# Optimization experiments

Hardware: AMD Instinct MI355X
Metric: run time of the kernel (lower is better)

The kernel has to match this reference:

```python
import jax, jax.numpy as jnp
import numpy as np
from jax import lax

# dims per init_kwargs / input_specs
V, D, N, W, B, T = 32000, 512, 250000, 64, 4, 1024
LOOPS, THRESH = 4, 0.99


def _ln(x, scale, bias):
    m = jnp.mean(x, -1, keepdims=True)
    v = jnp.var(x, -1, keepdims=True)
    return (x - m) * lax.rsqrt(v + 1e-5) * scale + bias


def setup_inputs() -> dict:
    key = jax.random.key(0)
    ks = jax.random.split(key, 12)
    s = 0.02
    p = lambda k, shape: jax.random.normal(k, shape, jnp.float32) * s
    return {
        "input_ids": jax.random.randint(ks[0], (B, T), 0, V),
        "embed": p(ks[1], (V, D)),
        "enc_w": p(ks[2], (D, D)), "enc_b": jnp.zeros((D,), jnp.float32),
        "ln_enc_s": jnp.ones((D,), jnp.float32), "ln_enc_b": jnp.zeros((D,), jnp.float32),
        "idx_w": p(ks[3], (D, D)), "idx_b": jnp.zeros((D,), jnp.float32),
        "mu_w": p(ks[4], (D, 1)), "mu_b": jnp.zeros((1,), jnp.float32),
        "sig_w": p(ks[5], (D, 1)), "sig_b": jnp.zeros((1,), jnp.float32),
        "pool_table": p(ks[6], (N, D)),
        "int_w1": p(ks[7], (2 * D, D)), "int_b1": jnp.zeros((D,), jnp.float32),
        "int_w2": p(ks[8], (D, D)), "int_b2": jnp.zeros((D,), jnp.float32),
        "ln_s": jnp.ones((D,), jnp.float32), "ln_b": jnp.zeros((D,), jnp.float32),
        "halt_w": p(ks[9], (D, 1)), "halt_b": jnp.zeros((1,), jnp.float32),
        "dec_w": p(ks[10], (D, V)), "dec_b": jnp.zeros((V,), jnp.float32),
    }


def reference(input_ids, embed, enc_w, enc_b, ln_enc_s, ln_enc_b,
              idx_w, idx_b, mu_w, mu_b, sig_w, sig_b, pool_table,
              int_w1, int_b1, int_w2, int_b2, ln_s, ln_b,
              halt_w, halt_b, dec_w, dec_b):
    # TinyController.encode: embed -> Dense -> gelu -> LayerNorm
    hidden = _ln(jax.nn.gelu(embed[input_ids] @ enc_w + enc_b), ln_enc_s, ln_enc_b)  # [B,T,D]
    state = hidden
    dt = hidden.dtype
    halt_prob = jnp.zeros((B, T, 1), dt)
    halted = jnp.zeros((B, T, 1), dt)
    idxs = []
    for _ in range(LOOPS):  # fixed small loop count, unrolled
        prev = state
        pooled = jnp.mean(state, axis=1)                       # [B,D]
        h = jax.nn.gelu(pooled @ idx_w + idx_b)
        mu = jax.nn.sigmoid(h @ mu_w + mu_b)                   # [B,1], coord in [0,1]
        sigma = jax.nn.softplus(h @ sig_w + sig_b) + 1e-4      # [B,1]
        # CoordinateMassivePool: contiguous window of W rows around mu*N
        center = mu[:, 0] * N
        start = jnp.clip(jnp.floor(center - W / 2).astype(jnp.int32), 0, N - W)  # [B]
        window = jax.vmap(lambda s: lax.dynamic_slice(pool_table, (s, 0), (W, D)))(start)  # [B,W,D]
        pos = (start[:, None] + jnp.arange(W)[None, :]).astype(dt) / N            # [B,W]
        w = jnp.exp(-0.5 * ((pos - mu) / sigma) ** 2)
        w = w / jnp.sum(w, axis=-1, keepdims=True)
        retrieved = jnp.einsum('bw,bwd->bd', w, window)        # [B,D]
        combined = jnp.concatenate(
            [state, jnp.broadcast_to(retrieved[:, None, :], (B, T, D))], axis=-1)  # [B,T,2D]
        integrated = _ln(jax.nn.gelu(combined @ int_w1 + int_b1) @ int_w2 + int_b2, ln_s, ln_b)
        candidate = state + integrated
        # ACT halting
        p_halt = jax.nn.sigmoid(candidate @ halt_w + halt_b)   # [B,T,1]
        halt_prob = halt_prob + p_halt * (1.0 - halted)
        new_halted = (halt_prob > THRESH).astype(dt)
        state = (1.0 - halted) * candidate + halted * prev
        halted = new_halted
        idxs.append(start)
    logits = state @ dec_w + dec_b                             # [B,T,V]
    all_indices = jnp.stack(idxs, axis=1)                      # [B,LOOPS]
    return logits, all_indices
```

## Files before the change

kernel.cpp:

```cpp
#include <hip/hip_runtime.h>

#define DEV __device__ __forceinline__

typedef __attribute__((ext_vector_type(8))) short bf16x8;
typedef __attribute__((ext_vector_type(4))) float f32x4;

typedef const __attribute__((address_space(1))) void* gsrc_t;
typedef __attribute__((address_space(3))) void* gdst_t;

DEV void gld16(const void* g, void* l){ __builtin_amdgcn_global_load_lds((gsrc_t)g,(gdst_t)l,16,0,0); }

DEV unsigned short f2bf(float f){
  union { float f; unsigned int u; } x; x.f = f;
  unsigned int u = x.u;
  return (unsigned short)((u + 0x7fffu + ((u >> 16) & 1u)) >> 16);
}
DEV unsigned long long pack4bf(float a, float b, float c, float d){
  return (unsigned long long)f2bf(a)
       | ((unsigned long long)f2bf(b) << 16)
       | ((unsigned long long)f2bf(c) << 32)
       | ((unsigned long long)f2bf(d) << 48);
}
DEV float gelu_t(float x){
  float u = 0.7978845608028654f * (x + 0.044715f * x * x * x);
  return 0.5f * x * (1.0f + tanhf(u));
}
DEV float sigmoidf_(float x){ return 1.0f / (1.0f + expf(-x)); }

DEV void BAR_TOP(){ __builtin_amdgcn_s_barrier(); asm volatile("" ::: "memory"); }
DEV void BAR_END(){
  __builtin_amdgcn_sched_barrier(0);
  asm volatile("s_waitcnt lgkmcnt(0)" ::: "memory");
  __builtin_amdgcn_s_barrier();
  asm volatile("" ::: "memory");
}

__global__ __launch_bounds__(256) void kPrep(const float* __restrict__ dec_w,
                                             unsigned short* __restrict__ dec_wT,
                                             const float* __restrict__ s0, const float* __restrict__ s1,
                                             const float* __restrict__ s2,
                                             unsigned short* __restrict__ d0, unsigned short* __restrict__ d1,
                                             unsigned short* __restrict__ d2,
                                             const int* __restrict__ ids,
                                             const float* __restrict__ embed,
                                             unsigned short* __restrict__ E){
  __shared__ float t[64][65];
  const int bid = blockIdx.x, tid = threadIdx.x;
  if (bid < 4000){
    int n0 = (bid % 500) * 64, k0 = (bid / 500) * 64;
    #pragma unroll
    for (int i = 0; i < 16; i++){
      int idx = i * 256 + tid; int r = idx >> 6, c = idx & 63;
      t[r][c] = dec_w[(size_t)(k0 + r) * 32000 + n0 + c];
    }
    __syncthreads();
    #pragma unroll
    for (int i = 0; i < 16; i++){
      int idx = i * 256 + tid; int r = idx >> 6, c = idx & 63;
      dec_wT[(size_t)(n0 + r) * 512 + k0 + c] = f2bf(t[c][r]);
    }
  } else if (bid < 4192){
    int rel = bid - 4000;
    int z = rel >> 6, rem = rel & 63;
    const float* W = (z == 0) ? s0 : (z == 1) ? s1 : s2;
    unsigned short* D = (z == 0) ? d0 : (z == 1) ? d1 : d2;
    int n0 = (rem & 7) * 64, k0 = (rem >> 3) * 64;
    #pragma unroll
    for (int i = 0; i < 16; i++){
      int idx = i * 256 + tid; int r = idx >> 6, c = idx & 63;
      t[r][c] = W[(size_t)(k0 + r) * 512 + n0 + c];
    }
    __syncthreads();
    #pragma unroll
    for (int i = 0; i < 16; i++){
      int idx = i * 256 + tid; int r = idx >> 6, c = idx & 63;
      D[(size_t)(n0 + r) * 512 + k0 + c] = f2bf(t[c][r]);
    }
  } else {
    int idx = bid - 4192;
    int row = idx * 2 + (tid >> 7);
    int t2  = tid & 127;
    int id = ids[row];
    float4 v = ((const float4*)(embed + (size_t)id * 512))[t2];
    *(unsigned long long*)(E + (size_t)row * 512 + t2 * 4) = pack4bf(v.x, v.y, v.z, v.w);
  }
}

template<int ENC>
__global__ __launch_bounds__(512) void kGemmLN(
    const unsigned short* __restrict__ A, const unsigned short* __restrict__ BT,
    const float* __restrict__ bias, const float* __restrict__ lns, const float* __restrict__ lnb,
    const float* __restrict__ hw, const float* __restrict__ hb,
    float* __restrict__ st, unsigned short* __restrict__ stb,
    float* __restrict__ part, float* __restrict__ halt_p, float* __restrict__ halted){
  __shared__ alignas(16) unsigned short lA[2][16 * 32];
  __shared__ alignas(16) unsigned short lB[2][512 * 32];
  __shared__ float pS[8][16], pQ[8][16], pH[8][16];
  __shared__ float sMean[16], sRs[16], sFac[16];
  const int tid = threadIdx.x, w = tid >> 6, lane = tid & 63;
  const int q = lane >> 4, c = lane & 15, lk8 = q * 8;
  const int r0 = blockIdx.x * 16;
  const int br = tid >> 2, bk = (tid & 3) * 8;
  f32x4 acc[4] = {};

  auto STAGE = [&](int buf, int k0){
    if (w == 0)
      gld16(A + (size_t)(r0 + (lane >> 2)) * 512 + k0 + (lane & 3) * 8, &lA[buf][lane * 8]);
    #pragma unroll
    for (int i = 0; i < 4; i++)
      gld16(BT + (size_t)(i * 128 + br) * 512 + k0 + bk, &lB[buf][(i * 512 + tid) * 8]);
  };

  STAGE(0, 0);
  #pragma unroll
  for (int t = 0; t < 16; t++){
    if (t < 15){
      STAGE((t + 1) & 1, (t + 1) * 32);
      if (w == 0) asm volatile("s_waitcnt vmcnt(5)" ::: "memory");
      else        asm volatile("s_waitcnt vmcnt(4)" ::: "memory");
    } else {
      asm volatile("s_waitcnt vmcnt(0)" ::: "memory");
    }
    BAR_TOP();
    bf16x8 af = *(const bf16x8*)&lA[t & 1][c * 32 + lk8];
    bf16x8 bfv[4];
    #pragma unroll
    for (int n = 0; n < 4; n++)
      bfv[n] = *(const bf16x8*)&lB[t & 1][(w * 64 + n * 16 + c) * 32 + lk8];
    #pragma unroll
    for (int n = 0; n < 4; n++)
      acc[n] = __builtin_amdgcn_mfma_f32_16x16x32_bf16(af, bfv[n], acc[n], 0, 0, 0);
    BAR_END();
  }

  #pragma unroll
  for (int n = 0; n < 4; n++){
    float bcol = bias[w * 64 + n * 16 + c];
    #pragma unroll
    for (int r = 0; r < 4; r++){
      float v = acc[n][r] + bcol;
      if (ENC) v = gelu_t(v);
      acc[n][r] = v;
    }
  }
  float rS[4], rQ[4];
  #pragma unroll
  for (int r = 0; r < 4; r++){
    float s = 0.f, s2 = 0.f;
    #pragma unroll
    for (int n = 0; n < 4; n++){ float v = acc[n][r]; s += v; s2 += v * v; }
    rS[r] = s; rQ[r] = s2;
  }
  #pragma unroll
  for (int mask = 1; mask < 16; mask <<= 1)
    #pragma unroll
    for (int r = 0; r < 4; r++){
      rS[r] += __shfl_xor(rS[r], mask);
      rQ[r] += __shfl_xor(rQ[r], mask);
    }
  if (c == 0)
    #pragma unroll
    for (int r = 0; r < 4; r++){ pS[w][q * 4 + r] = rS[r]; pQ[w][q * 4 + r] = rQ[r]; }
  __syncthreads();
  if (tid < 16){
    float s = 0.f, s2 = 0.f;
    #pragma unroll
    for (int v = 0; v < 8; v++){ s += pS[v][tid]; s2 += pQ[v][tid]; }
    float mean = s * (1.f / 512.f);
    float var  = s2 * (1.f / 512.f) - mean * mean;
    sMean[tid] = mean; sRs[tid] = rsqrtf(var + 1e-5f);
    if (ENC){ halt_p[r0 + tid] = 0.f; halted[r0 + tid] = 0.f; }
  }
  __syncthreads();
  float lnsv[4], lnbv[4];
  #pragma unroll
  for (int n = 0; n < 4; n++){ lnsv[n] = lns[w * 64 + n * 16 + c]; lnbv[n] = lnb[w * 64 + n * 16 + c]; }
  #pragma unroll
  for (int r = 0; r < 4; r++){
    int row = q * 4 + r;
    float mu = sMean[row], rs = sRs[row];
    #pragma unroll
    for (int n = 0; n < 4; n++)
      acc[n][r] = (acc[n][r] - mu) * rs * lnsv[n] + lnbv[n];
  }

  float sold[4][4];
  if (!ENC){
    float hwv[4];
    #pragma unroll
    for (int n = 0; n < 4; n++) hwv[n] = hw[w * 64 + n * 16 + c];
    #pragma unroll
    for (int r = 0; r < 4; r++){
      int row = q * 4 + r;
      #pragma unroll
      for (int n = 0; n < 4; n++)
        sold[n][r] = st[(size_t)(r0 + row) * 512 + w * 64 + n * 16 + c];
    }
    float rH[4];
    #pragma unroll
    for (int r = 0; r < 4; r++){
      float d = 0.f;
      #pragma unroll
      for (int n = 0; n < 4; n++) d += (sold[n][r] + acc[n][r]) * hwv[n];
      rH[r] = d;
    }
    #pragma unroll
    for (int mask = 1; mask < 16; mask <<= 1)
      #pragma unroll
      for (int r = 0; r < 4; r++) rH[r] += __shfl_xor(rH[r], mask);
    if (c == 0)
      #pragma unroll
      for (int r = 0; r < 4; r++) pH[w][q * 4 + r] = rH[r];
    __syncthreads();
    if (tid < 16){
      float d = 0.f;
      #pragma unroll
      for (int v = 0; v < 8; v++) d += pH[v][tid];
      float hd = halted[r0 + tid];
      float p  = sigmoidf_(d + hb[0]);
      float hp = halt_p[r0 + tid] + p * (1.f - hd);
      halt_p[r0 + tid] = hp;
      halted[r0 + tid] = (hp > 0.99f) ? 1.f : 0.f;
      sFac[tid] = 1.f - hd;
    }
    __syncthreads();
    #pragma unroll
    for (int r = 0; r < 4; r++){
      float f = sFac[q * 4 + r];
      #pragma unroll
      for (int n = 0; n < 4; n++)
        acc[n][r] = sold[n][r] + f * acc[n][r];
    }
  }

  #pragma unroll
  for (int r = 0; r < 4; r++){
    int row = r0 + q * 4 + r;
    #pragma unroll
    for (int n = 0; n < 4; n++){
      int col = w * 64 + n * 16 + c;
      float v = acc[n][r];
      st [(size_t)row * 512 + col] = v;
      stb[(size_t)row * 512 + col] = f2bf(v);
    }
  }
  #pragma unroll
  for (int n = 0; n < 4; n++){
    float s = 0.f;
    #pragma unroll
    for (int r = 0; r < 4; r++) s += acc[n][r];
    s += __shfl_xor(s, 16);
    s += __shfl_xor(s, 32);
    if (q == 0) part[(size_t)blockIdx.x * 512 + w * 64 + n * 16 + c] = s;
  }
}

__global__ __launch_bounds__(256) void kGemm64(const unsigned short* __restrict__ A,
                                               const unsigned short* __restrict__ BT,
                                               const float* __restrict__ rb,
                                               unsigned short* __restrict__ C){
  __shared__ alignas(16) unsigned short lA[2][64 * 32];
  __shared__ alignas(16) unsigned short lB[2][64 * 32];
  const int tid = threadIdx.x, w = tid >> 6, lane = tid & 63;
  const int q = lane >> 4, c = lane & 15, lk8 = q * 8;
  const int wm = w >> 1, wn = w & 1;
  const int m0 = blockIdx.y * 64, n0 = blockIdx.x * 64;
  const int sr = tid >> 2, sk = (tid & 3) * 8;
  f32x4 acc[2][2] = {};

  auto STAGE = [&](int buf, int k0){
    gld16(A  + (size_t)(m0 + sr) * 512 + k0 + sk, &lA[buf][tid * 8]);
    gld16(BT + (size_t)(n0 + sr) * 512 + k0 + sk, &lB[buf][tid * 8]);
  };

  STAGE(0, 0);
  #pragma unroll
  for (int t = 0; t < 16; t++){
    if (t < 15){
      STAGE((t + 1) & 1, (t + 1) * 32);
      asm volatile("s_waitcnt vmcnt(2)" ::: "memory");
    } else {
      asm volatile("s_waitcnt vmcnt(0)" ::: "memory");
    }
    BAR_TOP();
    bf16x8 af[2], bfv[2];
    #pragma unroll
    for (int m = 0; m < 2; m++) af[m]  = *(const bf16x8*)&lA[t & 1][(wm * 32 + m * 16 + c) * 32 + lk8];
    #pragma unroll
    for (int n = 0; n < 2; n++) bfv[n] = *(const bf16x8*)&lB[t & 1][(wn * 32 + n * 16 + c) * 32 + lk8];
    #pragma unroll
    for (int m = 0; m < 2; m++)
      #pragma unroll
      for (int n = 0; n < 2; n++)
        acc[m][n] = __builtin_amdgcn_mfma_f32_16x16x32_bf16(af[m], bfv[n], acc[m][n], 0, 0, 0);
    BAR_END();
  }

  #pragma unroll
  for (int m = 0; m < 2; m++)
    #pragma unroll
    for (int n = 0; n < 2; n++)
      #pragma unroll
      for (int r = 0; r < 4; r++){
        int row = m0 + wm * 32 + m * 16 + q * 4 + r;
        int col = n0 + wn * 32 + n * 16 + c;
        float v = acc[m][n][r] + rb[((row >> 10) << 9) + col];
        C[(size_t)row * 512 + col] = f2bf(gelu_t(v));
      }
}

__global__ __launch_bounds__(512) void kGemmDec(const unsigned short* __restrict__ A,
                                                const unsigned short* __restrict__ BT,
                                                const float* __restrict__ bias,
                                                float* __restrict__ C){
  __shared__ alignas(16) unsigned short lA[3][128 * 32];
  __shared__ alignas(16) unsigned short lB[3][256 * 32];
  const int tid = threadIdx.x, w = tid >> 6, lane = tid & 63;
  const int wm = w >> 2, wn = w & 3;
  const int c = lane & 15, q = lane >> 4;
  const int rk8 = (q ^ ((c >> 1) & 3)) * 8;
  int flat = blockIdx.x;
  flat = (flat & 7) * 500 + (flat >> 3);
  const int m0 = (flat & 31) * 128;
  const int n0 = (flat >> 5) * 256;
  const int srow  = tid >> 2;
  const int skoff = ((tid & 3) ^ ((srow >> 1) & 3)) * 8;
  const int sdst  = srow * 32 + (tid & 3) * 8;
  f32x4 acc[4][4] = {};

  auto STAGE = [&](int buf, int k0){
    gld16(A  + (size_t)(m0 + srow) * 512 + k0 + skoff,       &lA[buf][sdst]);
    gld16(BT + (size_t)(n0 + srow) * 512 + k0 + skoff,       &lB[buf][sdst]);
    gld16(BT + (size_t)(n0 + 128 + srow) * 512 + k0 + skoff, &lB[buf][128 * 32 + sdst]);
  };

  STAGE(0, 0);
  STAGE(1, 32);
  for (int t = 0; t < 16; t++){
    const int buf = t % 3;
    if (t < 15) asm volatile("s_waitcnt vmcnt(3)" ::: "memory");
    else        asm volatile("s_waitcnt vmcnt(0)" ::: "memory");
    __builtin_amdgcn_s_barrier();
    asm volatile("" ::: "memory");
    if (t < 14) STAGE((t + 2) % 3, (t + 2) * 32);
    bf16x8 af[4], bfr[4];
    #pragma unroll
    for (int mf = 0; mf < 4; mf++)
      af[mf] = *(const bf16x8*)&lA[buf][(wm * 64 + mf * 16 + c) * 32 + rk8];
    #pragma unroll
    for (int nf = 0; nf < 4; nf++)
      bfr[nf] = *(const bf16x8*)&lB[buf][(wn * 64 + nf * 16 + c) * 32 + rk8];
    __builtin_amdgcn_s_setprio(1);
    #pragma unroll
    for (int mf = 0; mf < 4; mf++)
      #pragma unroll
      for (int nf = 0; nf < 4; nf++)
        acc[mf][nf] = __builtin_amdgcn_mfma_f32_16x16x32_bf16(af[mf], bfr[nf], acc[mf][nf], 0, 0, 0);
    __builtin_amdgcn_s_setprio(0);
  }

  #pragma unroll
  for (int mf = 0; mf < 4; mf++){
    int rbase = m0 + wm * 64 + mf * 16 + q * 4;
    #pragma unroll
    for (int nf = 0; nf < 4; nf++){
      int col = n0 + wn * 64 + nf * 16 + c;
      float bcol = bias[col];
      #pragma unroll
      for (int r = 0; r < 4; r++)
        __builtin_nontemporal_store(acc[mf][nf][r] + bcol,
                                    &C[(size_t)(rbase + r) * 32000 + col]);
    }
  }
}

__global__ __launch_bounds__(512) void kCtl(const float* __restrict__ part,
                                            const float* __restrict__ idx_w, const float* __restrict__ idx_b,
                                            const float* __restrict__ mu_w, const float* __restrict__ mu_b,
                                            const float* __restrict__ sig_w, const float* __restrict__ sig_b,
                                            const float* __restrict__ pool_table,
                                            const float* __restrict__ w1b, const float* __restrict__ int_b1,
                                            float* __restrict__ r2, float* __restrict__ outIdx, int loop){
  __shared__ float xs[512];
  __shared__ float red[512];
  __shared__ float red2[512];
  __shared__ float evals[64];
  __shared__ float sc[4];
  int b = blockIdx.x, tid = threadIdx.x;

  float s = 0.f;
  #pragma unroll 8
  for (int c2 = 0; c2 < 64; c2++) s += part[(size_t)(b * 64 + c2) * 512 + tid];
  xs[tid] = s * (1.0f / 1024.0f);
  __syncthreads();

  float a = idx_b[tid];
  #pragma unroll 32
  for (int i = 0; i < 512; i++)
    a = fmaf(xs[i], idx_w[(size_t)i * 512 + tid], a);
  float hv = gelu_t(a);
  red[tid]  = hv * mu_w[tid];
  red2[tid] = hv * sig_w[tid];
  __syncthreads();
  for (int off2 = 256; off2 > 0; off2 >>= 1){
    if (tid < off2){ red[tid] += red[tid + off2]; red2[tid] += red2[tid + off2]; }
    __syncthreads();
  }
  if (tid == 0){
    float mu = sigmoidf_(red[0] + mu_b[0]);
    float sg = log1pf(expf(red2[0] + sig_b[0])) + 1e-4f;
    float center = mu * 250000.0f;
    int stt = (int)floorf(center - 32.0f);
    stt = stt < 0 ? 0 : (stt > 250000 - 64 ? 250000 - 64 : stt);
    sc[0] = mu; sc[1] = sg; sc[2] = (float)stt;
    outIdx[b * 4 + loop] = (float)stt;
  }
  __syncthreads();
  if (tid < 64){
    float pos = (sc[2] + (float)tid) * (1.0f / 250000.0f);
    float z = (pos - sc[0]) / sc[1];
    evals[tid] = expf(-0.5f * z * z);
  }
  __syncthreads();
  if (tid == 0){
    float wsum = 0.f;
    for (int j = 0; j < 64; j++) wsum += evals[j];
    sc[3] = wsum;
  }
  __syncthreads();
  int stt = (int)sc[2];
  float r = 0.f;
  #pragma unroll 8
  for (int j = 0; j < 64; j++)
    r = fmaf(evals[j], pool_table[(size_t)(stt + j) * 512 + tid], r);
  r /= sc[3];
  __syncthreads();
  xs[tid] = r;
  __syncthreads();
  float a2 = int_b1[tid];
  #pragma unroll 32
  for (int i = 0; i < 512; i++)
    a2 = fmaf(xs[i], w1b[(size_t)i * 512 + tid], a2);
  r2[(size_t)b * 512 + tid] = a2;
}

extern "C" void kernel_launch(void* const* d_in, const int* in_sizes, int n_in,
                              void* d_out, int out_size, void* d_ws, size_t ws_size,
                              hipStream_t stream){
  (void)in_sizes; (void)n_in; (void)out_size; (void)ws_size;
  const int*   ids    = (const int*)  d_in[0];
  const float* embed  = (const float*)d_in[1];
  const float* enc_w  = (const float*)d_in[2];
  const float* enc_b  = (const float*)d_in[3];
  const float* ln_es  = (const float*)d_in[4];
  const float* ln_eb  = (const float*)d_in[5];
  const float* idx_w  = (const float*)d_in[6];
  const float* idx_b  = (const float*)d_in[7];
  const float* mu_w   = (const float*)d_in[8];
  const float* mu_b   = (const float*)d_in[9];
  const float* sig_w  = (const float*)d_in[10];
  const float* sig_b  = (const float*)d_in[11];
  const float* pool_t = (const float*)d_in[12];
  const float* int_w1 = (const float*)d_in[13];
  const float* int_b1 = (const float*)d_in[14];
  const float* int_w2 = (const float*)d_in[15];
  const float* int_b2 = (const float*)d_in[16];
  const float* ln_s   = (const float*)d_in[17];
  const float* ln_b   = (const float*)d_in[18];
  const float* halt_w = (const float*)d_in[19];
  const float* halt_b = (const float*)d_in[20];
  const float* dec_w  = (const float*)d_in[21];
  const float* dec_b  = (const float*)d_in[22];

  char* ws = (char*)d_ws;
  size_t off = 0;
  auto alloc = [&](size_t bytes)->char*{
    char* p = ws + off; off += (bytes + 255) & ~(size_t)255; return p;
  };
  unsigned short* dec_wT  = (unsigned short*)alloc(32000ull * 512 * 2);
  unsigned short* enc_wT  = (unsigned short*)alloc(512ull * 512 * 2);
  unsigned short* w1T     = (unsigned short*)alloc(512ull * 512 * 2);
  unsigned short* w2T     = (unsigned short*)alloc(512ull * 512 * 2);
  unsigned short* bufB    = (unsigned short*)alloc(4096ull * 512 * 2);
  float*          state   = (float*)alloc(4096ull * 512 * 4);
  unsigned short* state_b = (unsigned short*)alloc(4096ull * 512 * 2);
  float*          part    = (float*)alloc(256ull * 512 * 4);
  float*          r2      = (float*)alloc(4ull * 512 * 4);
  float*          halt_p  = (float*)alloc(4096 * 4);
  float*          halted  = (float*)alloc(4096 * 4);
  float*          outF    = (float*)d_out;

  hipLaunchKernelGGL(kPrep, dim3(6240), dim3(256), 0, stream,
                     dec_w, dec_wT, enc_w, int_w1, int_w2, enc_wT, w1T, w2T,
                     ids, embed, bufB);

  hipLaunchKernelGGL((kGemmLN<1>), dim3(256), dim3(512), 0, stream,
                     bufB, enc_wT, enc_b, ln_es, ln_eb,
                     (const float*)nullptr, (const float*)nullptr,
                     state, state_b, part, halt_p, halted);

  for (int l = 0; l < 4; l++){
    hipLaunchKernelGGL(kCtl, dim3(4), dim3(512), 0, stream, part, idx_w, idx_b,
                       mu_w, mu_b, sig_w, sig_b, pool_t,
                       int_w1 + 512 * 512, int_b1,
                       r2, outF + 131072000, l);
    hipLaunchKernelGGL(kGemm64, dim3(8, 64), dim3(256), 0, stream,
                       state_b, w1T, r2, bufB);
    hipLaunchKernelGGL((kGemmLN<0>), dim3(256), dim3(512), 0, stream,
                       bufB, w2T, int_b2, ln_s, ln_b, halt_w, halt_b,
                       state, state_b, part, halt_p, halted);
  }

  hipLaunchKernelGGL(kGemmDec, dim3(4000), dim3(512), 0, stream,
                     state_b, dec_wT, dec_b, (float*)d_out);
}
```

Before: 482.4 us.

## Triple-buffer LDS staging in GEMM kernels with one barrier per step

Switches kGemmLN and kGemm64 from double- to triple-buffered LDS staging with a prefetch distance of two tiles. This removes the second per-iteration barrier and the lgkmcnt drain. The next-next tile load is now issued after the single barrier, which is meant to hide global-load latency better and cut synchronisation cost. In exchange it uses more LDS, which may lower occupancy, and it drops full unrolling, so `t % 3` indexing and branch overhead appear. The vmcnt counts assume two stages are in flight, which is fragile if the compiler reorders loads.

After: 487.3 us. No clear change (+1.0%).

```diff
diff --git a/kernel.cpp b/kernel.cpp
--- a/kernel.cpp
+++ b/kernel.cpp
@@ -27,13 +27,7 @@
 }
 DEV float sigmoidf_(float x){ return 1.0f / (1.0f + expf(-x)); }
 
-DEV void BAR_TOP(){ __builtin_amdgcn_s_barrier(); asm volatile("" ::: "memory"); }
-DEV void BAR_END(){
-  __builtin_amdgcn_sched_barrier(0);
-  asm volatile("s_waitcnt lgkmcnt(0)" ::: "memory");
-  __builtin_amdgcn_s_barrier();
-  asm volatile("" ::: "memory");
-}
+DEV void BARRIER(){ __builtin_amdgcn_s_barrier(); asm volatile("" ::: "memory"); }
 
 __global__ __launch_bounds__(256) void kPrep(const float* __restrict__ dec_w,
                                              unsigned short* __restrict__ dec_wT,
@@ -93,8 +87,8 @@
     const float* __restrict__ hw, const float* __restrict__ hb,
     float* __restrict__ st, unsigned short* __restrict__ stb,
     float* __restrict__ part, float* __restrict__ halt_p, float* __restrict__ halted){
-  __shared__ alignas(16) unsigned short lA[2][16 * 32];
-  __shared__ alignas(16) unsigned short lB[2][512 * 32];
+  __shared__ alignas(16) unsigned short lA[3][16 * 32];
+  __shared__ alignas(16) unsigned short lB[3][512 * 32];
   __shared__ float pS[8][16], pQ[8][16], pH[8][16];
   __shared__ float sMean[16], sRs[16], sFac[16];
   const int tid = threadIdx.x, w = tid >> 6, lane = tid & 63;
@@ -112,25 +106,25 @@
   };
 
   STAGE(0, 0);
-  #pragma unroll
+  STAGE(1, 32);
   for (int t = 0; t < 16; t++){
+    const int buf = t % 3;
     if (t < 15){
-      STAGE((t + 1) & 1, (t + 1) * 32);
       if (w == 0) asm volatile("s_waitcnt vmcnt(5)" ::: "memory");
       else        asm volatile("s_waitcnt vmcnt(4)" ::: "memory");
     } else {
       asm volatile("s_waitcnt vmcnt(0)" ::: "memory");
     }
-    BAR_TOP();
-    bf16x8 af = *(const bf16x8*)&lA[t & 1][c * 32 + lk8];
+    BARRIER();
+    if (t < 14) STAGE((t + 2) % 3, (t + 2) * 32);
+    bf16x8 af = *(const bf16x8*)&lA[buf][c * 32 + lk8];
     bf16x8 bfv[4];
     #pragma unroll
     for (int n = 0; n < 4; n++)
-      bfv[n] = *(const bf16x8*)&lB[t & 1][(w * 64 + n * 16 + c) * 32 + lk8];
+      bfv[n] = *(const bf16x8*)&lB[buf][(w * 64 + n * 16 + c) * 32 + lk8];
     #pragma unroll
     for (int n = 0; n < 4; n++)
       acc[n] = __builtin_amdgcn_mfma_f32_16x16x32_bf16(af, bfv[n], acc[n], 0, 0, 0);
-    BAR_END();
   }
 
   #pragma unroll
@@ -259,8 +253,8 @@
                                                const unsigned short* __restrict__ BT,
                                                const float* __restrict__ rb,
                                                unsigned short* __restrict__ C){
-  __shared__ alignas(16) unsigned short lA[2][64 * 32];
-  __shared__ alignas(16) unsigned short lB[2][64 * 32];
+  __shared__ alignas(16) unsigned short lA[3][64 * 32];
+  __shared__ alignas(16) unsigned short lB[3][64 * 32];
   const int tid = threadIdx.x, w = tid >> 6, lane = tid & 63;
   const int q = lane >> 4, c = lane & 15, lk8 = q * 8;
   const int wm = w >> 1, wn = w & 1;
@@ -274,26 +268,23 @@
   };
 
   STAGE(0, 0);
-  #pragma unroll
+  STAGE(1, 32);
   for (int t = 0; t < 16; t++){
-    if (t < 15){
-      STAGE((t + 1) & 1, (t + 1) * 32);
-      asm volatile("s_waitcnt vmcnt(2)" ::: "memory");
-    } else {
-      asm volatile("s_waitcnt vmcnt(0)" ::: "memory");
-    }
-    BAR_TOP();
+    const int buf = t % 3;
+    if (t < 15) asm volatile("s_waitcnt vmcnt(2)" ::: "memory");
+    else        asm volatile("s_waitcnt vmcnt(0)" ::: "memory");
+    BARRIER();
+    if (t < 14) STAGE((t + 2) % 3, (t + 2) * 32);
     bf16x8 af[2], bfv[2];
     #pragma unroll
-    for (int m = 0; m < 2; m++) af[m]  = *(const bf16x8*)&lA[t & 1][(wm * 32 + m * 16 + c) * 32 + lk8];
-    #pragma unroll
-    for (int n = 0; n < 2; n++) bfv[n] = *(const bf16x8*)&lB[t & 1][(wn * 32 + n * 16 + c) * 32 + lk8];
+    for (int m = 0; m < 2; m++) af[m]  = *(const bf16x8*)&lA[buf][(wm * 32 + m * 16 + c) * 32 + lk8];
+    #pragma unroll
+    for (int n = 0; n < 2; n++) bfv[n] = *(const bf16x8*)&lB[buf][(wn * 32 + n * 16 + c) * 32 + lk8];
     #pragma unroll
     for (int m = 0; m < 2; m++)
       #pragma unroll
       for (int n = 0; n < 2; n++)
         acc[m][n] = __builtin_amdgcn_mfma_f32_16x16x32_bf16(af[m], bfv[n], acc[m][n], 0, 0, 0);
-    BAR_END();
   }
 
   #pragma unroll
```
